# Kernel tuning notes

Hardware: AMD Instinct MI355X
Metric: run time of the kernel (lower is better)

## Reference

```python
import jax, jax.numpy as jnp
import numpy as np

B, N, C = 4, 2048, 1152
H = 16
DH = C // H  # 72
EPS = 1e-6
THETA = 10000.0


def _rms_norm(x, w):
    # per-head RMSNorm in fp32, matching LlamaRMSNorm
    xf = x.astype(jnp.float32)
    var = jnp.mean(xf * xf, axis=-1, keepdims=True)
    return (w * (xf * jax.lax.rsqrt(var + EPS)).astype(x.dtype))


def _rope_cos_sin(n, dh, dtype):
    half = dh // 2
    inv_freq = 1.0 / (THETA ** (jnp.arange(0, half, dtype=jnp.float32) / half))
    ang = jnp.arange(n, dtype=jnp.float32)[:, None] * inv_freq[None, :]  # [N, half]
    return jnp.cos(ang).astype(dtype), jnp.sin(ang).astype(dtype)


def _apply_rope(x, cos, sin):
    # x: [B,H,N,DH]; rotate-half style
    half = x.shape[-1] // 2
    x1, x2 = x[..., :half], x[..., half:]
    return jnp.concatenate([x1 * cos - x2 * sin, x2 * cos + x1 * sin], axis=-1)


def setup_inputs() -> dict:
    key = jax.random.key(0)
    ks = jax.random.split(key, 3)
    x = jax.random.normal(ks[0], (B, N, C), dtype=jnp.float32)
    w_qkv = jax.random.normal(ks[1], (3 * C, C), dtype=jnp.float32) * (C ** -0.5)
    w_proj = jax.random.normal(ks[2], (C, C), dtype=jnp.float32) * (C ** -0.5)
    b_proj = jnp.zeros((C,), dtype=jnp.float32)
    q_norm_w = jnp.ones((DH,), dtype=jnp.float32)
    k_norm_w = jnp.ones((DH,), dtype=jnp.float32)
    return {"x": x, "w_qkv": w_qkv, "w_proj": w_proj, "b_proj": b_proj,
            "q_norm_w": q_norm_w, "k_norm_w": k_norm_w}


def reference(x, w_qkv, w_proj, b_proj, q_norm_w, k_norm_w):
    b, n, c = x.shape
    # QKV projection (no bias)
    qkv = jnp.einsum('bnc,dc->bnd', x, w_qkv)  # [B,N,3C]
    qkv = qkv.reshape(b, n, 3, H, DH).transpose(2, 0, 3, 1, 4)  # [3,B,H,N,DH]
    q, k, v = qkv[0], qkv[1], qkv[2]
    # RoPE on q, k
    cos, sin = _rope_cos_sin(n, DH, x.dtype)  # [N, DH/2]
    q = _apply_rope(q, cos, sin)
    k = _apply_rope(k, cos, sin)
    # per-head QK RMSNorm
    q = _rms_norm(q, q_norm_w)
    k = _rms_norm(k, k_norm_w)
    # scaled dot-product attention
    scale = DH ** -0.5
    attn = jax.nn.softmax(jnp.einsum('bhqd,bhkd->bhqk', q, k) * scale, axis=-1)
    out = jnp.einsum('bhqk,bhkd->bhqd', attn, v)  # [B,H,N,DH]
    out = out.transpose(0, 2, 1, 3).reshape(b, n, c)
    return jnp.einsum('bnc,dc->bnd', out, w_proj) + b_proj
```

## Files before the change

### kernel.cpp

```cpp
#include <hip/hip_runtime.h>
#include <stdint.h>

#define BATCH 4
#define NSEQ  2048
#define CDIM  1152
#define HB    16
#define DHD   72
#define D3    3456
#define NT    8192

typedef __attribute__((ext_vector_type(8))) short short8;
typedef __attribute__((ext_vector_type(8))) unsigned short u16x8;
typedef __attribute__((ext_vector_type(4))) unsigned short u16x4;
typedef __attribute__((ext_vector_type(2))) unsigned int u32x2;
typedef __attribute__((ext_vector_type(4))) float f32x4;

__device__ __forceinline__ float bf2f(unsigned short u) {
  return __uint_as_float(((unsigned)u) << 16);
}
__device__ __forceinline__ unsigned short f2bf(float f) {
  unsigned u = __float_as_uint(f);
  u += 0x7FFF + ((u >> 16) & 1);
  return (unsigned short)(u >> 16);
}
__device__ __forceinline__ unsigned pkbf(float lo, float hi) {
  unsigned r;
  asm("v_cvt_pk_bf16_f32 %0, %1, %2" : "=v"(r) : "v"(lo), "v"(hi));
  return r;
}
__device__ __forceinline__ float exp2_raw(float x) {
  float r;
  asm("v_exp_f32 %0, %1" : "=v"(r) : "v"(x));
  return r;
}

__device__ __forceinline__ void gload_lds16(const unsigned short* g, unsigned short* l) {
  __builtin_amdgcn_global_load_lds(
      (const __attribute__((address_space(1))) void*)g,
      (__attribute__((address_space(3))) void*)l, 16, 0, 0);
}

#define XN    ((size_t)NT * CDIM)
#define WQN   ((size_t)D3 * CDIM)
#define WPN   ((size_t)CDIM * CDIM)
#define CVT_CHUNKS ((XN + WQN + WPN) / 4)

__global__ __launch_bounds__(256) void cvt_bf16(
    const float* __restrict__ x, const float* __restrict__ wq,
    const float* __restrict__ wp, unsigned short* __restrict__ xb,
    unsigned short* __restrict__ wqb, unsigned short* __restrict__ wpb) {
  size_t c = (size_t)blockIdx.x * 256 + threadIdx.x;
  if (c >= CVT_CHUNKS) return;
  const float* src;
  unsigned short* dst;
  size_t e = c * 4;
  if (e < XN) { src = x + e; dst = xb + e; }
  else if (e < XN + WQN) { src = wq + (e - XN); dst = wqb + (e - XN); }
  else { src = wp + (e - XN - WQN); dst = wpb + (e - XN - WQN); }
  f32x4 v = *(const f32x4*)src;
  u16x4 r;
#pragma unroll
  for (int i = 0; i < 4; i++) r[i] = f2bf(v[i]);
  *(u16x4*)dst = r;
}

__global__ __launch_bounds__(512, 2) void gemm256_qkv(
    const unsigned short* __restrict__ A, const unsigned short* __restrict__ Bt,
    unsigned short* __restrict__ qkvb, unsigned short* __restrict__ Vt) {
  __shared__ __attribute__((aligned(16))) unsigned short sA[2 * 256 * 64];
  __shared__ __attribute__((aligned(16))) unsigned short sB[2 * 256 * 64];

  const int K = CDIM;
  const int tid  = threadIdx.x;
  const int lane = tid & 63;
  const int w    = tid >> 6;
  const int wm   = w >> 2, wn = w & 3;
  const int quad = lane >> 4, l16 = lane & 15;
  const int s7l  = l16 & 7;

  const int lb  = blockIdx.y * gridDim.x + blockIdx.x;
  const int xcd = lb & 7;
  const int pos = lb >> 3;
  const int m0 = (xcd * 4 + (pos & 3)) * 256;
  const int n0 = (pos >> 2) * 256;

  const int r8 = lane >> 3;
  const int cu = (lane & 7) ^ r8;
  const unsigned short* gA = A  + (size_t)(m0 + w * 8 + r8) * K + cu * 8;
  const unsigned short* gB = Bt + (size_t)(n0 + w * 8 + r8) * K + cu * 8;

  const f32x4 zero = {0.f, 0.f, 0.f, 0.f};
  f32x4 acc[8][4];
#pragma unroll
  for (int i = 0; i < 8; i++)
#pragma unroll
    for (int j = 0; j < 4; j++) acc[i][j] = zero;

#pragma unroll
  for (int g = 0; g < 4; g++) {
    gload_lds16(gA + (size_t)g * 64 * K, sA + g * 4096 + w * 512);
    gload_lds16(gB + (size_t)g * 64 * K, sB + g * 4096 + w * 512);
  }
  __syncthreads();

  for (int t = 0; t < 18; t++) {
    const unsigned short* A_ = sA + (t & 1) * 16384;
    const unsigned short* B_ = sB + (t & 1) * 16384;
    unsigned short* An = sA + ((t + 1) & 1) * 16384;
    unsigned short* Bn = sB + ((t + 1) & 1) * 16384;
    const int ktn = (t + 1) * 64;

#pragma unroll
    for (int kk = 0; kk < 2; kk++) {
      short8 a[8], b[4];
#pragma unroll
      for (int i = 0; i < 8; i++)
        a[i] = *(const short8*)(A_ + (wm * 128 + i * 16 + l16) * 64 +
                                (((kk * 4 + quad) ^ s7l) << 3));
#pragma unroll
      for (int j = 0; j < 4; j++)
        b[j] = *(const short8*)(B_ + (wn * 64 + j * 16 + l16) * 64 +
                                (((kk * 4 + quad) ^ s7l) << 3));

      if (t < 17) {
#pragma unroll
        for (int g = 0; g < 4; g++) {
          if (kk == 0)
            gload_lds16(gA + (size_t)g * 64 * K + ktn, An + g * 4096 + w * 512);
          else
            gload_lds16(gB + (size_t)g * 64 * K + ktn, Bn + g * 4096 + w * 512);
        }
      }

      __builtin_amdgcn_s_setprio(1);
#pragma unroll
      for (int i = 0; i < 8; i++)
#pragma unroll
        for (int j = 0; j < 4; j++)
          acc[i][j] = __builtin_amdgcn_mfma_f32_16x16x32_bf16(a[i], b[j], acc[i][j], 0, 0, 0);
      __builtin_amdgcn_s_setprio(0);
    }
    __syncthreads();
  }

#pragma unroll
  for (int i = 0; i < 8; i++) {
    int row = m0 + wm * 128 + i * 16 + quad * 4;
    int b_ = row >> 11;
    int n  = row & 2047;
#pragma unroll
    for (int j = 0; j < 4; j++) {
      int col = n0 + wn * 64 + j * 16 + l16;
      if (col < D3) {
        int s  = col / CDIM;
        int rm = col - s * CDIM;
        int h  = rm / DHD;
        int dh = rm - h * DHD;
        if (s == 2) {
#pragma unroll
          for (int r = 0; r < 4; r++)
            Vt[((size_t)(b_ * HB + h) * DHD + dh) * NSEQ + n + r] = f2bf(acc[i][j][r]);
        } else {
#pragma unroll
          for (int r = 0; r < 4; r++)
            qkvb[(((size_t)(s * BATCH + b_) * HB + h) * NSEQ + (n + r)) * DHD + dh] =
                f2bf(acc[i][j][r]);
        }
      }
    }
  }
}

__global__ __launch_bounds__(256) void gemm_bt(
    const unsigned short* __restrict__ A, const unsigned short* __restrict__ Bt,
    const float* __restrict__ bias, float* __restrict__ Cout, int M, int Dn, int K) {
  __shared__ __attribute__((aligned(16))) unsigned short sA[128 * 64];
  __shared__ __attribute__((aligned(16))) unsigned short sB[128 * 64];

  const int tid  = threadIdx.x;
  const int lane = tid & 63;
  const int w    = tid >> 6;
  const int wm   = w >> 1, wn = w & 1;
  const int quad = lane >> 4, l16 = lane & 15;
  const int s7l  = l16 & 7;

  const int gx  = gridDim.x;
  const int lb  = blockIdx.y * gx + blockIdx.x;
  const int xcd = lb & 7;
  const int pos = lb >> 3;
  const int m0 = ((xcd << 3) + (pos & 7)) * 128;
  const int n0 = (pos >> 3) * 128;

  const int r8 = lane >> 3;
  const int cu = (lane & 7) ^ r8;
  const unsigned short* gA = A  + (size_t)(m0 + w * 32 + r8) * K + cu * 8;
  const unsigned short* gB = Bt + (size_t)(n0 + w * 32 + r8) * K + cu * 8;

  const f32x4 zero = {0.f, 0.f, 0.f, 0.f};
  f32x4 acc[4][4];
#pragma unroll
  for (int i = 0; i < 4; i++)
#pragma unroll
    for (int j = 0; j < 4; j++) acc[i][j] = zero;

  for (int kt = 0; kt < K; kt += 64) {
#pragma unroll
    for (int i = 0; i < 4; i++) {
      gload_lds16(gA + (size_t)i * 8 * K + kt, sA + (w * 4 + i) * 512);
      gload_lds16(gB + (size_t)i * 8 * K + kt, sB + (w * 4 + i) * 512);
    }
    __syncthreads();

#pragma unroll
    for (int kk = 0; kk < 2; kk++) {
      short8 a[4], b[4];
#pragma unroll
      for (int i = 0; i < 4; i++) {
        a[i] = *(const short8*)(sA + (wm * 64 + i * 16 + l16) * 64 +
                                (((kk * 4 + quad) ^ s7l) << 3));
        b[i] = *(const short8*)(sB + (wn * 64 + i * 16 + l16) * 64 +
                                (((kk * 4 + quad) ^ s7l) << 3));
      }
#pragma unroll
      for (int i = 0; i < 4; i++)
#pragma unroll
        for (int j = 0; j < 4; j++)
          acc[i][j] = __builtin_amdgcn_mfma_f32_16x16x32_bf16(a[i], b[j], acc[i][j], 0, 0, 0);
    }
    __syncthreads();
  }

#pragma unroll
  for (int i = 0; i < 4; i++) {
    int row = m0 + wm * 64 + i * 16 + quad * 4;
#pragma unroll
    for (int j = 0; j < 4; j++) {
      int col = n0 + wn * 64 + j * 16 + l16;
      float bb = bias ? bias[col] : 0.f;
#pragma unroll
      for (int r = 0; r < 4; r++)
        Cout[(size_t)(row + r) * Dn + col] = acc[i][j][r] + bb;
    }
  }
}

__global__ __launch_bounds__(256) void rope_rms(
    unsigned short* __restrict__ qkvb,
    const float* __restrict__ qw, const float* __restrict__ kw) {
  const int blk = blockIdx.x;
  const int b = blk >> 11;
  const int n = blk & 2047;
  const int tid = threadIdx.x;

  __shared__ float sv[2][CDIM];
  __shared__ float srsq[2][HB];

  const float nf = (float)n;
  const float l2t_over_half = 13.287712379549449f / 36.0f;
  const float scale2 = 0.17002329230297715f;

  for (int g = tid; g < 288; g += 256) {
    int sel = (g >= 144) ? 1 : 0;
    int gg  = g - sel * 144;
    int h   = gg / 9;
    int u   = gg - h * 9;
    const unsigned short* src =
        qkvb + (((size_t)(sel * BATCH + b) * HB + h) * NSEQ + n) * DHD + u * 8;
    u16x8 v = *(const u16x8*)src;
    float* dst = &sv[sel][h * DHD + u * 8];
#pragma unroll
    for (int r = 0; r < 8; r++) dst[r] = bf2f(v[r]);
  }
  __syncthreads();

  for (int p = tid; p < 1152; p += 256) {
    int sel = (p >= 576) ? 1 : 0;
    int pp  = p - sel * 576;
    int h   = pp / 36;
    int i   = pp - h * 36;
    float* row = &sv[sel][h * DHD];
    float x1 = row[i], x2 = row[i + 36];
    float ang = nf * exp2f(-l2t_over_half * (float)i);
    float sn, cs;
    __sincosf(ang, &sn, &cs);
    row[i]      = x1 * cs - x2 * sn;
    row[i + 36] = x2 * cs + x1 * sn;
  }
  __syncthreads();

  if (tid < 128) {
    int sel = tid >> 6;
    int h = (tid & 63) >> 2, p = tid & 3;
    float s = 0.f;
#pragma unroll
    for (int d = 0; d < 18; d++) {
      float v = sv[sel][h * DHD + p * 18 + d];
      s += v * v;
    }
    s += __shfl_xor(s, 1);
    s += __shfl_xor(s, 2);
    if (p == 0)
      srsq[sel][h] = rsqrtf(s * (1.0f / 72.0f) + 1e-6f) * (sel ? 1.0f : scale2);
  }
  __syncthreads();

  for (int g = tid; g < 288; g += 256) {
    int sel = (g >= 144) ? 1 : 0;
    int gg  = g - sel * 144;
    int h   = gg / 9;
    int u   = gg - h * 9;
    float rs = srsq[sel][h];
    const float* wn = (sel ? kw : qw) + u * 8;
    const float* s = &sv[sel][h * DHD + u * 8];
    u16x8 o;
#pragma unroll
    for (int r = 0; r < 8; r++) o[r] = f2bf(s[r] * rs * wn[r]);
    unsigned short* dst =
        qkvb + (((size_t)(sel * BATCH + b) * HB + h) * NSEQ + n) * DHD + u * 8;
    *(u16x8*)dst = o;
  }
}

__global__ __launch_bounds__(512, 4) void flash_attn(
    const unsigned short* __restrict__ qkvb, const unsigned short* __restrict__ Vt,
    unsigned short* __restrict__ AO) {
  __shared__ __attribute__((aligned(16))) unsigned short sK[64 * 72];
  __shared__ __attribute__((aligned(16))) unsigned short sVt[80 * 64];
  __shared__ __attribute__((aligned(16))) unsigned short sP[256 * 64];

  const int tid  = threadIdx.x;
  const int w    = tid >> 6;
  const int lane = tid & 63;
  const int quad = lane >> 4, l16 = lane & 15;
  const int s7   = l16 & 7;
  const int q0 = blockIdx.x * 256;
  const int h = blockIdx.y, b = blockIdx.z;

  const unsigned short* Qb = qkvb + ((size_t)(0 * BATCH + b) * HB + h) * NSEQ * DHD;
  const unsigned short* Kb = qkvb + ((size_t)(1 * BATCH + b) * HB + h) * NSEQ * DHD;
  const unsigned short* Vb = Vt + (size_t)(b * HB + h) * DHD * NSEQ;

  const short8 zs = {0, 0, 0, 0, 0, 0, 0, 0};
  const f32x4 zero = {0.f, 0.f, 0.f, 0.f};

  const int vswz = ((lane & 7) ^ (lane >> 3)) * 8;
  const unsigned short* pKn[2];
  const unsigned short* pVn[2];
#pragma unroll
  for (int j = 0; j < 2; j++) {
    int i = w + 8 * j;
    int ii = (i < 9) ? i : 0;
    pKn[j] = Kb + ii * 512 + lane * 8;
    pVn[j] = Vb + (size_t)(ii * 8 + (lane >> 3)) * NSEQ + vswz;
  }

#pragma unroll
  for (int j = 0; j < 2; j++) {
    int i = w + 8 * j;
    if (i < 9) {
      gload_lds16(pKn[j], sK + i * 512);
      gload_lds16(pVn[j], sVt + i * 512);
      pKn[j] += 64 * 72;
      pVn[j] += 64;
    }
  }

  {
    int e = tid;
    sVt[72 * 64 + e] = (e < 64) ? (unsigned short)0x3F80 : (unsigned short)0;
  }

  short8 aq[2][3];
#pragma unroll
  for (int qt = 0; qt < 2; qt++) {
    const unsigned short* qrow = Qb + (size_t)(q0 + w * 32 + qt * 16 + l16) * DHD;
    aq[qt][0] = *(const short8*)(qrow + quad * 8);
    aq[qt][1] = *(const short8*)(qrow + 32 + quad * 8);
    aq[qt][2] = (quad == 0) ? *(const short8*)(qrow + 64) : zs;
  }

  f32x4 o[2][5];
#pragma unroll
  for (int qt = 0; qt < 2; qt++)
#pragma unroll
    for (int nb = 0; nb < 5; nb++) o[qt][nb] = zero;

  auto sphase_pack = [&]() {
    f32x4 st[2][4];
    __builtin_amdgcn_s_setprio(1);
#pragma unroll
    for (int nk = 0; nk < 4; nk++) {
      const unsigned short* kr = sK + (nk * 16 + l16) * 72;
      short8 kf0 = *(const short8*)(kr + quad * 8);
      short8 kf1 = *(const short8*)(kr + 32 + quad * 8);
      short8 kf2 = *(const short8*)(kr + 64);
      f32x4 s0 = zero, s1 = zero;
      s0 = __builtin_amdgcn_mfma_f32_16x16x32_bf16(kf0, aq[0][0], s0, 0, 0, 0);
      s1 = __builtin_amdgcn_mfma_f32_16x16x32_bf16(kf0, aq[1][0], s1, 0, 0, 0);
      s0 = __builtin_amdgcn_mfma_f32_16x16x32_bf16(kf1, aq[0][1], s0, 0, 0, 0);
      s1 = __builtin_amdgcn_mfma_f32_16x16x32_bf16(kf1, aq[1][1], s1, 0, 0, 0);
      s0 = __builtin_amdgcn_mfma_f32_16x16x32_bf16(kf2, aq[0][2], s0, 0, 0, 0);
      s1 = __builtin_amdgcn_mfma_f32_16x16x32_bf16(kf2, aq[1][2], s1, 0, 0, 0);
      st[0][nk] = s0;
      st[1][nk] = s1;
    }
    __builtin_amdgcn_s_setprio(0);
#pragma unroll
    for (int qt = 0; qt < 2; qt++) {
      unsigned short* prow = sP + (qt * 128 + w * 16 + l16) * 64 + (quad & 1) * 4;
#pragma unroll
      for (int nk = 0; nk < 4; nk++) {
        int uoff = ((nk * 2 + (quad >> 1)) ^ s7) << 3;
        u32x2 pr;
        pr[0] = pkbf(exp2_raw(st[qt][nk][0]), exp2_raw(st[qt][nk][1]));
        pr[1] = pkbf(exp2_raw(st[qt][nk][2]), exp2_raw(st[qt][nk][3]));
        *(u32x2*)(prow + uoff) = pr;
      }
    }
  };

  auto pv_phase = [&]() {
    __builtin_amdgcn_s_setprio(1);
#pragma unroll
    for (int kb = 0; kb < 2; kb++) {
      const unsigned short* pp =
          sP + (w * 16 + l16) * 64 + (((kb * 4 + quad) ^ s7) << 3);
      short8 pf0 = *(const short8*)pp;
      short8 pf1 = *(const short8*)(pp + 128 * 64);
#pragma unroll
      for (int nb = 0; nb < 5; nb++) {
        short8 vf = *(const short8*)(sVt + (nb * 16 + l16) * 64 +
                                     (((kb * 4 + quad) ^ s7) << 3));
        o[0][nb] = __builtin_amdgcn_mfma_f32_16x16x32_bf16(pf0, vf, o[0][nb], 0, 0, 0);
        o[1][nb] = __builtin_amdgcn_mfma_f32_16x16x32_bf16(pf1, vf, o[1][nb], 0, 0, 0);
      }
    }
    __builtin_amdgcn_s_setprio(0);
  };

  __syncthreads();

  for (int t = 0; t < 32; t++) {
    sphase_pack();

    __syncthreads();

    if (t < 31) {
#pragma unroll
      for (int j = 0; j < 2; j++) {
        int i = w + 8 * j;
        if (i < 9) { gload_lds16(pKn[j], sK + i * 512); pKn[j] += 64 * 72; }
      }
    }

    pv_phase();

    __syncthreads();

    if (t < 31) {
#pragma unroll
      for (int j = 0; j < 2; j++) {
        int i = w + 8 * j;
        if (i < 9) { gload_lds16(pVn[j], sVt + i * 512); pVn[j] += 64; }
      }
    }
  }

#pragma unroll
  for (int qt = 0; qt < 2; qt++) {
    float inv[4];
#pragma unroll
    for (int r = 0; r < 4; r++)
      inv[r] = 1.0f / __shfl(o[qt][4][r], (quad << 4) + 8, 64);
    const int qrow = q0 + w * 32 + qt * 16 + quad * 4;
#pragma unroll
    for (int nb = 0; nb < 5; nb++) {
      int dh = nb * 16 + l16;
      if (dh < DHD) {
#pragma unroll
        for (int r = 0; r < 4; r++)
          AO[((size_t)b * NSEQ + qrow + r) * CDIM + h * DHD + dh] =
              f2bf(o[qt][nb][r] * inv[r]);
      }
    }
  }
}

extern "C" void kernel_launch(void* const* d_in, const int* in_sizes, int n_in,
                              void* d_out, int out_size, void* d_ws, size_t ws_size,
                              hipStream_t stream) {
  const float* x      = (const float*)d_in[0];
  const float* w_qkv  = (const float*)d_in[1];
  const float* w_proj = (const float*)d_in[2];
  const float* b_proj = (const float*)d_in[3];
  const float* qnw    = (const float*)d_in[4];
  const float* knw    = (const float*)d_in[5];
  float* out = (float*)d_out;

  char* ws = (char*)d_ws;
  unsigned short* xb    = (unsigned short*)(ws);
  unsigned short* wqkvb = (unsigned short*)(ws + 18874368);
  unsigned short* wprojb= (unsigned short*)(ws + 26836992);
  unsigned short* qkvb  = (unsigned short*)(ws + 29491200);
  unsigned short* Vt    = (unsigned short*)(ws + 67239936);
  unsigned short* AO    = xb;

  cvt_bf16<<<dim3((CVT_CHUNKS + 255) / 256), 256, 0, stream>>>(
      x, w_qkv, w_proj, xb, wqkvb, wprojb);
  gemm256_qkv<<<dim3(14, 32), 512, 0, stream>>>(xb, wqkvb, qkvb, Vt);
  rope_rms<<<dim3(NT), 256, 0, stream>>>(qkvb, qnw, knw);
  flash_attn<<<dim3(NSEQ / 256, HB, BATCH), 512, 0, stream>>>(qkvb, Vt, AO);
  gemm_bt<<<dim3(CDIM / 128, NT / 128), 256, 0, stream>>>(
      AO, wprojb, b_proj, out, NT, CDIM, CDIM);
}
```

Measured before the change: 323.2 us.

## Double-buffer K and V tiles in LDS and merge per-iteration barriers

Allocates two LDS buffers each for the K and V^T tiles. The next tile's K and V loads are issued at the start of each iteration into the alternate buffer, while the current buffers feed the QK^T and PV MFMA phases. This cuts the loop from two __syncthreads to one and lets global-to-LDS traffic overlap both compute phases. The cost is more LDS per block (about 72KB against about 52KB), which may reduce how many blocks fit on a CU.

```diff
diff --git a/kernel.cpp b/kernel.cpp
--- a/kernel.cpp
+++ b/kernel.cpp
@@ -324,8 +324,8 @@
 __global__ __launch_bounds__(512, 4) void flash_attn(
     const unsigned short* __restrict__ qkvb, const unsigned short* __restrict__ Vt,
     unsigned short* __restrict__ AO) {
-  __shared__ __attribute__((aligned(16))) unsigned short sK[64 * 72];
-  __shared__ __attribute__((aligned(16))) unsigned short sVt[80 * 64];
+  __shared__ __attribute__((aligned(16))) unsigned short sK[2 * 64 * 72];
+  __shared__ __attribute__((aligned(16))) unsigned short sVt[2 * 80 * 64];
   __shared__ __attribute__((aligned(16))) unsigned short sP[256 * 64];
 
   const int tid  = threadIdx.x;
@@ -367,7 +367,9 @@
 
   {
     int e = tid;
-    sVt[72 * 64 + e] = (e < 64) ? (unsigned short)0x3F80 : (unsigned short)0;
+    unsigned short v = (e < 64) ? (unsigned short)0x3F80 : (unsigned short)0;
+    sVt[72 * 64 + e] = v;
+    sVt[80 * 64 + 72 * 64 + e] = v;
   }
 
   short8 aq[2][3];
@@ -385,12 +387,12 @@
 #pragma unroll
     for (int nb = 0; nb < 5; nb++) o[qt][nb] = zero;
 
-  auto sphase_pack = [&]() {
+  auto sphase_pack = [&](const unsigned short* sKb) {
     f32x4 st[2][4];
     __builtin_amdgcn_s_setprio(1);
 #pragma unroll
     for (int nk = 0; nk < 4; nk++) {
-      const unsigned short* kr = sK + (nk * 16 + l16) * 72;
+      const unsigned short* kr = sKb + (nk * 16 + l16) * 72;
       short8 kf0 = *(const short8*)(kr + quad * 8);
       short8 kf1 = *(const short8*)(kr + 32 + quad * 8);
       short8 kf2 = *(const short8*)(kr + 64);
@@ -419,7 +421,7 @@
     }
   };
 
-  auto pv_phase = [&]() {
+  auto pv_phase = [&](const unsigned short* sVb) {
     __builtin_amdgcn_s_setprio(1);
 #pragma unroll
     for (int kb = 0; kb < 2; kb++) {
@@ -429,7 +431,7 @@
       short8 pf1 = *(const short8*)(pp + 128 * 64);
 #pragma unroll
       for (int nb = 0; nb < 5; nb++) {
-        short8 vf = *(const short8*)(sVt + (nb * 16 + l16) * 64 +
+        short8 vf = *(const short8*)(sVb + (nb * 16 + l16) * 64 +
                                      (((kb * 4 + quad) ^ s7) << 3));
         o[0][nb] = __builtin_amdgcn_mfma_f32_16x16x32_bf16(pf0, vf, o[0][nb], 0, 0, 0);
         o[1][nb] = __builtin_amdgcn_mfma_f32_16x16x32_bf16(pf1, vf, o[1][nb], 0, 0, 0);
@@ -441,29 +443,28 @@
   __syncthreads();
 
   for (int t = 0; t < 32; t++) {
-    sphase_pack();
-
-    __syncthreads();
+    const unsigned short* sKb = sK + (t & 1) * (64 * 72);
+    const unsigned short* sVb = sVt + (t & 1) * (80 * 64);
 
     if (t < 31) {
+      unsigned short* dK = sK + ((t + 1) & 1) * (64 * 72);
+      unsigned short* dV = sVt + ((t + 1) & 1) * (80 * 64);
 #pragma unroll
       for (int j = 0; j < 2; j++) {
         int i = w + 8 * j;
-        if (i < 9) { gload_lds16(pKn[j], sK + i * 512); pKn[j] += 64 * 72; }
-      }
-    }
-
-    pv_phase();
+        if (i < 9) {
+          gload_lds16(pKn[j], dK + i * 512);
+          gload_lds16(pVn[j], dV + i * 512);
+          pKn[j] += 64 * 72;
+          pVn[j] += 64;
+        }
+      }
+    }
+
+    sphase_pack(sKb);
+    pv_phase(sVb);
 
     __syncthreads();
-
-    if (t < 31) {
-#pragma unroll
-      for (int j = 0; j < 2; j++) {
-        int i = w + 8 * j;
-        if (i < 9) { gload_lds16(pVn[j], sVt + i * 512); pVn[j] += 64; }
-      }
-    }
   }
 
 #pragma unroll
```

After: 317.1 us. About the same (-1.9%).
